# Kernel optimization log

Hardware: AMD Instinct MI355X
Metric: run time of the kernel (lower is better)

## Reference

```python
import jax, jax.numpy as jnp
import numpy as np

N_NODES = 100000
N_EDGES = 1200000
D_IN = 64
D_OUT = 64


def setup_inputs() -> dict:
    key = jax.random.key(0)
    ks = jax.random.split(key, 8)
    feat = jax.random.normal(ks[0], (N_NODES, D_IN), dtype=jnp.float32)
    src = jax.random.randint(ks[1], (N_EDGES,), 0, N_NODES, dtype=jnp.int32)
    dst = jax.random.randint(ks[2], (N_EDGES,), 0, N_NODES, dtype=jnp.int32)
    edge_weight = jax.random.uniform(ks[3], (N_EDGES, 1), dtype=jnp.float32)
    edge_mask = jax.random.uniform(ks[4], (N_EDGES, 1), dtype=jnp.float32)
    W_self = jax.random.normal(ks[5], (D_OUT, D_IN), dtype=jnp.float32) * (1.0 / np.sqrt(D_IN))
    b_self = jnp.zeros((D_OUT,), dtype=jnp.float32)
    W_neigh = jax.random.normal(ks[6], (D_OUT, D_IN), dtype=jnp.float32) * (1.0 / np.sqrt(D_IN))
    b_neigh = jnp.zeros((D_OUT,), dtype=jnp.float32)
    return {"feat": feat, "src": src, "dst": dst, "edge_weight": edge_weight,
            "edge_mask": edge_mask, "W_self": W_self, "b_self": b_self,
            "W_neigh": W_neigh, "b_neigh": b_neigh}


def reference(feat, src, dst, edge_weight, edge_mask, W_self, b_self, W_neigh, b_neigh):
    # message: gather src feats, scale by per-edge weight and mask  -> [E, D_IN]
    msg = feat[src] * edge_weight * edge_mask
    # mean scatter-reduce over incoming edges per dst node
    neigh_sum = jax.ops.segment_sum(msg, dst, num_segments=N_NODES)  # [N, D_IN]
    deg = jax.ops.segment_sum(jnp.ones((msg.shape[0],), dtype=feat.dtype), dst,
                              num_segments=N_NODES)  # [N]
    h_neigh = neigh_sum / jnp.maximum(deg, 1.0)[:, None]  # zero-degree nodes -> 0 (DGL mean semantics)
    # dual linear fuse
    rst = (feat @ W_self.T + b_self) + (h_neigh @ W_neigh.T + b_neigh)
    return rst
```

## Files before the change

### kernel.cpp

```cpp
#include <hip/hip_runtime.h>

#define NB_MAX   1568
#define CAP      1024
#define BT_EDGES 4096
#define BT_TPB   1024
#define EPE      4

typedef __attribute__((ext_vector_type(4))) float floatx4;
typedef __attribute__((ext_vector_type(2))) float floatx2;
typedef __attribute__((ext_vector_type(8))) short bf16x8;

__device__ __forceinline__ unsigned short f32_to_bf16(float f) {
  unsigned u = __float_as_uint(f);
  u = (u + 0x7fffu + ((u >> 16) & 1u)) >> 16;
  return (unsigned short)u;
}
__device__ __forceinline__ unsigned pack2(float a, float b) {
  return (unsigned)f32_to_bf16(a) | ((unsigned)f32_to_bf16(b) << 16);
}
__device__ __forceinline__ bf16x8 zero_bf16x8() {
  bf16x8 v;
#pragma unroll
  for (int i = 0; i < 8; ++i) v[i] = 0;
  return v;
}

#if __has_builtin(__builtin_amdgcn_cvt_pk_fp8_f32)
__device__ __forceinline__ unsigned pack_fp8x4(float a, float b, float c, float d) {
  unsigned v = (unsigned)__builtin_amdgcn_cvt_pk_fp8_f32(a, b, 0, false);
  v = (unsigned)__builtin_amdgcn_cvt_pk_fp8_f32(c, d, (int)v, true);
  return v;
}
#else
__device__ __forceinline__ unsigned sw_f32_fp8(float f) {
  unsigned u = __float_as_uint(f);
  unsigned s = (u >> 24) & 0x80u;
  unsigned au = u & 0x7fffffffu;
  if (au > 0x43E00000u) au = 0x43E00000u;
  au += 0x7FFFFu + ((au >> 20) & 1u);
  int e = (int)(au >> 23) - 120;
  if (e <= 0) return s;
  return s | ((unsigned)e << 3) | ((au >> 20) & 7u);
}
__device__ __forceinline__ unsigned pack_fp8x4(float a, float b, float c, float d) {
  return sw_f32_fp8(a) | (sw_f32_fp8(b) << 8) | (sw_f32_fp8(c) << 16) |
         (sw_f32_fp8(d) << 24);
}
#endif

#if __has_builtin(__builtin_amdgcn_cvt_pk_f32_fp8)
__device__ __forceinline__ void dec4(float* acc, unsigned w32, float wt) {
  floatx2 f0 = __builtin_amdgcn_cvt_pk_f32_fp8((int)w32, false);
  floatx2 f1 = __builtin_amdgcn_cvt_pk_f32_fp8((int)w32, true);
  acc[0] += wt * f0.x; acc[1] += wt * f0.y;
  acc[2] += wt * f1.x; acc[3] += wt * f1.y;
}
#else
__device__ __forceinline__ float sw_fp8_f32(unsigned b) {
  unsigned s = (b & 0x80u) << 24;
  unsigned e = (b >> 3) & 0xFu;
  unsigned m = b & 7u;
  float fn = __uint_as_float(s | ((e + 120u) << 23) | (m << 20));
  float fd = (float)(int)m * 0.001953125f;
  fd = (b & 0x80u) ? -fd : fd;
  return e ? fn : fd;
}
__device__ __forceinline__ void dec4(float* acc, unsigned w32, float wt) {
  acc[0] += wt * sw_fp8_f32(w32 & 0xFF);
  acc[1] += wt * sw_fp8_f32((w32 >> 8) & 0xFF);
  acc[2] += wt * sw_fp8_f32((w32 >> 16) & 0xFF);
  acc[3] += wt * sw_fp8_f32(w32 >> 24);
}
#endif

__global__ __launch_bounds__(BT_TPB) void k_build(
    const float* __restrict__ feat, const int* __restrict__ src,
    const int* __restrict__ dst, const float* __restrict__ ew,
    const float* __restrict__ em, const float* __restrict__ Ws,
    const float* __restrict__ Wn, int* __restrict__ gCursor,
    unsigned* __restrict__ recs, unsigned short* __restrict__ featb,
    unsigned char* __restrict__ featq, unsigned short* __restrict__ Wb,
    int E, int nChunks, int nB) {
  __shared__ unsigned stage[BT_EDGES];
  __shared__ unsigned short stageB[BT_EDGES];
  __shared__ int A[NB_MAX];
  __shared__ int B[NB_MAX];
  __shared__ int waveSums[16];

  const int t = threadIdx.x;
  const int lane = t & 63;
  const int wvid = t >> 6;
  const int e0 = blockIdx.x * BT_EDGES;
  const int eEnd = min(e0 + BT_EDGES, E);
  const int nLocal = eEnd - e0;

  for (int i = t; i < NB_MAX; i += BT_TPB) B[i] = 0;
  __syncthreads();

  int dreg[EPE];
#pragma unroll
  for (int k = 0; k < EPE; ++k) {
    int i = e0 + k * BT_TPB + t;
    dreg[k] = -1;
    if (i < eEnd) {
      int d = dst[i];
      dreg[k] = d;
      atomicAdd(&B[d >> 6], 1);
    }
  }
  __syncthreads();

  {
    const int EPT = 2;
    int b0 = t * EPT;
    int v[EPT];
    int sum = 0;
#pragma unroll
    for (int j = 0; j < EPT; ++j) {
      v[j] = (b0 + j < nB) ? B[b0 + j] : 0;
      sum += v[j];
    }
    int x = sum;
#pragma unroll
    for (int d = 1; d < 64; d <<= 1) {
      int y = __shfl_up(x, d, 64);
      if (lane >= d) x += y;
    }
    if (lane == 63) waveSums[wvid] = x;
    __syncthreads();
    int wprefix = 0;
    for (int i = 0; i < wvid; ++i) wprefix += waveSums[i];
    int run = wprefix + x - sum;
#pragma unroll
    for (int j = 0; j < EPT; ++j) {
      if (b0 + j < nB) A[b0 + j] = run;
      run += v[j];
    }
  }
  __syncthreads();

  for (int i = t; i < nB; i += BT_TPB) {
    int c = B[i];
    int l = A[i];
    int g = c ? atomicAdd(&gCursor[i], c) : 0;
    A[i] = i * CAP + g - l;
    B[i] = l;
  }
  __syncthreads();

#pragma unroll
  for (int k = 0; k < EPE; ++k) {
    int i = e0 + k * BT_TPB + t;
    if (i < eEnd) {
      int d = dreg[k];
      int bkt = d >> 6;
      int r = atomicAdd(&B[bkt], 1);
      float w = ew[i] * em[i];
      int wq = (int)(w * 511.0f + 0.5f);
      if (wq > 511) wq = 511;
      stage[r] = (unsigned)src[i] | ((unsigned)(d & 63) << 17) |
                 ((unsigned)wq << 23);
      stageB[r] = (unsigned short)bkt;
    }
  }
  __syncthreads();

  for (int i = t; i < nLocal; i += BT_TPB) {
    int bkt = stageB[i];
    int pos = A[bkt] + i;
    if (pos < (bkt + 1) * CAP)
      recs[pos] = stage[i];
  }

  for (int c = blockIdx.x * BT_TPB + t; c < nChunks; c += gridDim.x * BT_TPB) {
    const float4* fp = reinterpret_cast<const float4*>(feat) + (size_t)c * 2;
    float4 a = fp[0], b = fp[1];
    uint4 o;
    o.x = pack2(a.x, a.y);
    o.y = pack2(a.z, a.w);
    o.z = pack2(b.x, b.y);
    o.w = pack2(b.z, b.w);
    reinterpret_cast<uint4*>(featb)[c] = o;
    uint2 q8;
    q8.x = pack_fp8x4(a.x, a.y, a.z, a.w);
    q8.y = pack_fp8x4(b.x, b.y, b.z, b.w);
    reinterpret_cast<uint2*>(featq)[c] = q8;
  }

  if (blockIdx.x == 0) {
    for (int i = t; i < 1024; i += BT_TPB) {
      int j = i >> 4, c4 = i & 15;
      float4 w4 = reinterpret_cast<const float4*>(Ws)[i];
      float4 n4 = reinterpret_cast<const float4*>(Wn)[i];
      *reinterpret_cast<uint2*>(&Wb[j * 128 + c4 * 4]) =
          make_uint2(pack2(w4.x, w4.y), pack2(w4.z, w4.w));
      *reinterpret_cast<uint2*>(&Wb[j * 128 + 64 + c4 * 4]) =
          make_uint2(pack2(n4.x, n4.y), pack2(n4.z, n4.w));
    }
  }
}

__global__ __launch_bounds__(512) void sage_gather_gemm(
    const unsigned short* __restrict__ featb,
    const unsigned char* __restrict__ featq,
    const unsigned short* __restrict__ Wb, const int* __restrict__ gCursor,
    const unsigned* __restrict__ recs, const float* __restrict__ bs,
    const float* __restrict__ bn, float* __restrict__ out, int N) {
  __shared__ unsigned short An[64][72];
  __shared__ unsigned rawL[CAP];
  __shared__ unsigned srtL[CAP];
  __shared__ float pf[64][64];
  __shared__ int cntS[64], offS[64], curS[64];

  const int t = threadIdx.x;
  const int b = blockIdx.x;
  const int n0 = b * 64;
  const int base = b * CAP;
  const int cb = min(gCursor[b], CAP);

  for (int i = t; i < cb; i += 512) rawL[i] = recs[base + i];
  if (t < 64) cntS[t] = 0;
  __syncthreads();

  for (int i = t; i < cb; i += 512)
    atomicAdd(&cntS[(rawL[i] >> 17) & 63], 1);
  __syncthreads();

  if (t < 64) {
    int c = cntS[t];
    int x = c;
#pragma unroll
    for (int d = 1; d < 64; d <<= 1) {
      int y = __shfl_up(x, d, 64);
      if (t >= d) x += y;
    }
    offS[t] = x - c;
    curS[t] = x - c;
  }
  __syncthreads();

  for (int i = t; i < cb; i += 512) {
    unsigned r = rawL[i];
    int p = atomicAdd(&curS[(r >> 17) & 63], 1);
    srtL[p] = r;
  }
  __syncthreads();

  {
    const int nl = t >> 3;
    const int g  = (t >> 2) & 1;
    const int q  = t & 3;
    const int deg = cntS[nl], off = offS[nl];
    const int myN = (deg - g + 1) >> 1;
    float acc[16];
#pragma unroll
    for (int i = 0; i < 16; ++i) acc[i] = 0.f;
    const uint4* fq = reinterpret_cast<const uint4*>(featq);

    uint4 uC, uN;
    float wC = 0.f, wN = 0.f;
    if (myN > 0) {
      unsigned r0 = srtL[off + g];
      uC = fq[(size_t)(r0 & 0x1FFFF) * 4 + q];
      wC = (float)(r0 >> 23) * (1.0f / 511.0f);
    }
    if (myN > 1) {
      unsigned r1 = srtL[off + g + 2];
      uN = fq[(size_t)(r1 & 0x1FFFF) * 4 + q];
      wN = (float)(r1 >> 23) * (1.0f / 511.0f);
    }
    for (int m = 0; m < myN; ++m) {
      uint4 u = uC;
      float w = wC;
      uC = uN; wC = wN;
      if (m + 2 < myN) {
        unsigned rn = srtL[off + g + 2 * (m + 2)];
        uN = fq[(size_t)(rn & 0x1FFFF) * 4 + q];
        wN = (float)(rn >> 23) * (1.0f / 511.0f);
      }
      dec4(acc + 0, u.x, w);
      dec4(acc + 4, u.y, w);
      dec4(acc + 8, u.z, w);
      dec4(acc + 12, u.w, w);
    }

    if (g == 1) {
#pragma unroll
      for (int i = 0; i < 16; ++i) pf[nl][q * 16 + i] = acc[i];
    }
    __syncthreads();
    if (g == 0) {
      float inv = 1.0f / fmaxf((float)deg, 1.0f);
#pragma unroll
      for (int i = 0; i < 16; ++i) acc[i] = (acc[i] + pf[nl][q * 16 + i]) * inv;
      uint4 o0, o1;
      o0.x = pack2(acc[0], acc[1]);
      o0.y = pack2(acc[2], acc[3]);
      o0.z = pack2(acc[4], acc[5]);
      o0.w = pack2(acc[6], acc[7]);
      o1.x = pack2(acc[8], acc[9]);
      o1.y = pack2(acc[10], acc[11]);
      o1.z = pack2(acc[12], acc[13]);
      o1.w = pack2(acc[14], acc[15]);
      *reinterpret_cast<uint4*>(&An[nl][q * 16]) = o0;
      *reinterpret_cast<uint4*>(&An[nl][q * 16 + 8]) = o1;
    }
  }
  __syncthreads();

  const int wv8 = t >> 6;
  const int nt = wv8 & 3;
  const int jh = wv8 >> 2;
  const int ln = t & 63;
  const int col = ln & 15;
  const int quad = ln >> 4;
  const int gn = n0 + nt * 16 + col;

  floatx4 acc4[2];
#pragma unroll
  for (int jj = 0; jj < 2; ++jj) {
    int jt = jh * 2 + jj;
    float bb = bs[jt * 16 + col] + bn[jt * 16 + col];
    acc4[jj] = (floatx4){bb, bb, bb, bb};
  }

#pragma unroll
  for (int kk = 0; kk < 4; ++kk) {
    bf16x8 af;
    if (kk < 2) {
      if (gn < N) {
        af = *reinterpret_cast<const bf16x8*>(featb + (size_t)gn * 64 + kk * 32 + quad * 8);
      } else {
        af = zero_bf16x8();
      }
    } else {
      af = *reinterpret_cast<const bf16x8*>(&An[nt * 16 + col][(kk - 2) * 32 + quad * 8]);
    }
#pragma unroll
    for (int jj = 0; jj < 2; ++jj) {
      int jt = jh * 2 + jj;
      bf16x8 bf = *reinterpret_cast<const bf16x8*>(
          Wb + (jt * 16 + col) * 128 + kk * 32 + quad * 8);
      acc4[jj] = __builtin_amdgcn_mfma_f32_16x16x32_bf16(af, bf, acc4[jj], 0, 0, 0);
    }
  }

#pragma unroll
  for (int jj = 0; jj < 2; ++jj) {
    int jt = jh * 2 + jj;
#pragma unroll
    for (int r = 0; r < 4; ++r) {
      int m = quad * 4 + r;
      int g2 = n0 + nt * 16 + m;
      if (g2 < N) out[(size_t)g2 * 64 + jt * 16 + col] = acc4[jj][r];
    }
  }
}

extern "C" void kernel_launch(void* const* d_in, const int* in_sizes, int n_in,
                              void* d_out, int out_size, void* d_ws, size_t ws_size,
                              hipStream_t stream) {
  const float* feat = (const float*)d_in[0];
  const int*   src  = (const int*)d_in[1];
  const int*   dst  = (const int*)d_in[2];
  const float* ew   = (const float*)d_in[3];
  const float* em   = (const float*)d_in[4];
  const float* Ws   = (const float*)d_in[5];
  const float* bs   = (const float*)d_in[6];
  const float* Wn   = (const float*)d_in[7];
  const float* bn   = (const float*)d_in[8];
  float* out = (float*)d_out;

  const int N = in_sizes[0] / 64;
  const int E = in_sizes[1];
  const int nB = (N + 63) / 64;

  unsigned short* featb = (unsigned short*)d_ws;
  unsigned char*  featq = (unsigned char*)(featb + (size_t)N * 64);
  unsigned short* Wb    = (unsigned short*)(featq + (size_t)N * 64);
  unsigned* recs   = (unsigned*)(Wb + 64 * 128);
  int*      gCursor = (int*)(recs + (size_t)NB_MAX * CAP);

  hipMemsetAsync(gCursor, 0, NB_MAX * sizeof(int), stream);

  int nChunks = N * 8;
  int gB = (E + BT_EDGES - 1) / BT_EDGES;

  k_build<<<gB, BT_TPB, 0, stream>>>(feat, src, dst, ew, em, Ws, Wn,
                                     gCursor, recs, featb, featq, Wb,
                                     E, nChunks, nB);
  sage_gather_gemm<<<nB, 512, 0, stream>>>(featb, featq, Wb, gCursor, recs,
                                           bs, bn, out, N);
}
```

Measured before the change: 161.2 us.

## Balance gather work by splitting sorted edges evenly across thread groups

Replaces the per-node assignment (eight threads per destination node, split into two halves) with an even split of the block's sorted edge list across 128 four-thread groups. Each group accumulates runs of edges that share a destination and flushes partial sums into a shared fp32 accumulator with LDS atomics whenever the node changes. A separate pass then normalizes by degree and packs to bf16. This targets load imbalance from skewed per-node degrees, at the cost of zeroing the shared accumulator, extra LDS atomics, and more shared memory, which may lower occupancy.

```diff
diff --git a/kernel.cpp b/kernel.cpp
--- a/kernel.cpp
+++ b/kernel.cpp
@@ -207,9 +207,9 @@
     const unsigned* __restrict__ recs, const float* __restrict__ bs,
     const float* __restrict__ bn, float* __restrict__ out, int N) {
   __shared__ unsigned short An[64][72];
+  __shared__ float accS[64][68];
   __shared__ unsigned rawL[CAP];
   __shared__ unsigned srtL[CAP];
-  __shared__ float pf[64][64];
   __shared__ int cntS[64], offS[64], curS[64];
 
   const int t = threadIdx.x;
@@ -218,6 +218,7 @@
   const int base = b * CAP;
   const int cb = min(gCursor[b], CAP);
 
+  for (int i = t; i < 64 * 68; i += 512) (&accS[0][0])[i] = 0.f;
   for (int i = t; i < cb; i += 512) rawL[i] = recs[base + i];
   if (t < 64) cntS[t] = 0;
   __syncthreads();
@@ -247,64 +248,80 @@
   __syncthreads();
 
   {
-    const int nl = t >> 3;
-    const int g  = (t >> 2) & 1;
-    const int q  = t & 3;
-    const int deg = cntS[nl], off = offS[nl];
-    const int myN = (deg - g + 1) >> 1;
+    const int gid = t >> 2;
+    const int q = t & 3;
+    const int chunk = (cb + 127) >> 7;
+    const int lo = gid * chunk;
+    const int hi = min(lo + chunk, cb);
+    const uint4* fq = reinterpret_cast<const uint4*>(featq);
+
     float acc[16];
 #pragma unroll
     for (int i = 0; i < 16; ++i) acc[i] = 0.f;
-    const uint4* fq = reinterpret_cast<const uint4*>(featq);
+    int curNode = -1;
 
     uint4 uC, uN;
     float wC = 0.f, wN = 0.f;
-    if (myN > 0) {
-      unsigned r0 = srtL[off + g];
+    int nC = -1, nN = -1;
+    if (lo < hi) {
+      unsigned r0 = srtL[lo];
       uC = fq[(size_t)(r0 & 0x1FFFF) * 4 + q];
       wC = (float)(r0 >> 23) * (1.0f / 511.0f);
-    }
-    if (myN > 1) {
-      unsigned r1 = srtL[off + g + 2];
+      nC = (r0 >> 17) & 63;
+    }
+    if (lo + 1 < hi) {
+      unsigned r1 = srtL[lo + 1];
       uN = fq[(size_t)(r1 & 0x1FFFF) * 4 + q];
       wN = (float)(r1 >> 23) * (1.0f / 511.0f);
-    }
-    for (int m = 0; m < myN; ++m) {
+      nN = (r1 >> 17) & 63;
+    }
+    for (int i = lo; i < hi; ++i) {
       uint4 u = uC;
       float w = wC;
-      uC = uN; wC = wN;
-      if (m + 2 < myN) {
-        unsigned rn = srtL[off + g + 2 * (m + 2)];
+      int node = nC;
+      uC = uN; wC = wN; nC = nN;
+      if (i + 2 < hi) {
+        unsigned rn = srtL[i + 2];
         uN = fq[(size_t)(rn & 0x1FFFF) * 4 + q];
         wN = (float)(rn >> 23) * (1.0f / 511.0f);
+        nN = (rn >> 17) & 63;
+      }
+      if (node != curNode) {
+        if (curNode >= 0) {
+#pragma unroll
+          for (int k = 0; k < 16; ++k) {
+            atomicAdd(&accS[curNode][q * 16 + k], acc[k]);
+            acc[k] = 0.f;
+          }
+        }
+        curNode = node;
       }
       dec4(acc + 0, u.x, w);
       dec4(acc + 4, u.y, w);
       dec4(acc + 8, u.z, w);
       dec4(acc + 12, u.w, w);
     }
-
-    if (g == 1) {
-#pragma unroll
-      for (int i = 0; i < 16; ++i) pf[nl][q * 16 + i] = acc[i];
-    }
-    __syncthreads();
-    if (g == 0) {
-      float inv = 1.0f / fmaxf((float)deg, 1.0f);
-#pragma unroll
-      for (int i = 0; i < 16; ++i) acc[i] = (acc[i] + pf[nl][q * 16 + i]) * inv;
-      uint4 o0, o1;
-      o0.x = pack2(acc[0], acc[1]);
-      o0.y = pack2(acc[2], acc[3]);
-      o0.z = pack2(acc[4], acc[5]);
-      o0.w = pack2(acc[6], acc[7]);
-      o1.x = pack2(acc[8], acc[9]);
-      o1.y = pack2(acc[10], acc[11]);
-      o1.z = pack2(acc[12], acc[13]);
-      o1.w = pack2(acc[14], acc[15]);
-      *reinterpret_cast<uint4*>(&An[nl][q * 16]) = o0;
-      *reinterpret_cast<uint4*>(&An[nl][q * 16 + 8]) = o1;
-    }
+    if (curNode >= 0) {
+#pragma unroll
+      for (int k = 0; k < 16; ++k)
+        atomicAdd(&accS[curNode][q * 16 + k], acc[k]);
+    }
+  }
+  __syncthreads();
+
+  {
+    int nl = t >> 3;
+    int part = t & 7;
+    float inv = 1.0f / fmaxf((float)cntS[nl], 1.0f);
+    const float* ap = &accS[nl][part * 8];
+    float4 a0 = *reinterpret_cast<const float4*>(ap);
+    float4 a1 = *reinterpret_cast<const float4*>(ap + 4);
+    uint4 o;
+    o.x = pack2(a0.x * inv, a0.y * inv);
+    o.y = pack2(a0.z * inv, a0.w * inv);
+    o.z = pack2(a1.x * inv, a1.y * inv);
+    o.w = pack2(a1.z * inv, a1.w * inv);
+    *reinterpret_cast<uint4*>(&An[nl][part * 8]) = o;
   }
   __syncthreads();
 
```

New measurement: 236.3 us. +46.5%, slower.
